# Performance work log

Measured on AMD Instinct MI355X. Metric: run time of the kernel, lower is better.

## Reference

```python
import jax, jax.numpy as jnp
import numpy as np

S, M, B, D, H, DH = 1024, 1024, 4, 1024, 16, 64
T = S + M
EPS = 1e-5


def setup_inputs() -> dict:
    key = jax.random.key(0)
    ks = jax.random.split(key, 6)
    x = jax.random.normal(ks[0], (S, B, D), dtype=jnp.float32)
    pos_emb = jax.random.normal(ks[1], (S, 1, D), dtype=jnp.float32)
    memory = jax.random.normal(ks[2], (M, B, D), dtype=jnp.float32)
    # causal mask: query i (global position M+i) cannot attend to key j > M+i
    i = jnp.arange(S)[:, None]
    j = jnp.arange(T)[None, :]
    mask = jnp.broadcast_to((j > (i + M))[:, :, None], (S, T, B))  # [S,T,B] bool
    w_qkv = jax.random.normal(ks[3], (D, 3 * H * DH), dtype=jnp.float32) * (D ** -0.5)
    w_o = jax.random.normal(ks[4], (H * DH, D), dtype=jnp.float32) * ((H * DH) ** -0.5)
    ln_gamma = jnp.ones((D,), dtype=jnp.float32)
    ln_beta = jnp.zeros((D,), dtype=jnp.float32)
    return {"x": x, "pos_emb": pos_emb, "memory": memory, "mask": mask,
            "w_qkv": w_qkv, "w_o": w_o, "ln_gamma": ln_gamma, "ln_beta": ln_beta}


def reference(x, pos_emb, memory, mask, w_qkv, w_o, ln_gamma, ln_beta):
    seq_len = x.shape[0]
    scale = 1.0 / (DH ** 0.5)
    x = x + pos_emb[-seq_len:]                      # [S,B,D]
    c = jnp.concatenate([memory, x], axis=0)        # [T,B,D]
    qkv = jnp.einsum('tbd,de->tbe', c, w_qkv)       # [T,B,3*H*DH]
    q, k, v = jnp.split(qkv, 3, axis=-1)
    q = q.reshape(-1, B, H, DH)[-seq_len:]          # [S,B,H,DH]
    k = k.reshape(-1, B, H, DH)                     # [T,B,H,DH]
    v = v.reshape(-1, B, H, DH)
    score = jnp.einsum('ibnd,jbnd->ijbn', q, k) * scale  # [S,T,B,H]
    score = jnp.where(mask[:, :, :, None], -jnp.inf, score)
    prob = jax.nn.softmax(score, axis=1)
    vec = jnp.einsum('ijbn,jbnd->ibnd', prob, v)    # [S,B,H,DH]
    vec = vec.reshape(seq_len, B, H * DH)
    attn_out = jnp.einsum('sbe,ed->sbd', vec, w_o)  # [S,B,D]
    y = x + attn_out
    mu = jnp.mean(y, axis=-1, keepdims=True)
    var = jnp.mean(jnp.square(y - mu), axis=-1, keepdims=True)
    out = (y - mu) * jax.lax.rsqrt(var + EPS) * ln_gamma + ln_beta
    return out
```

## Files before the change

### kernel.cpp

```cpp
#include <hip/hip_runtime.h>
#include <stdint.h>

#define S_  1024
#define M_  1024
#define B_  4
#define D_  1024
#define H_  16
#define DH_ 64
#define T_  2048

typedef __attribute__((ext_vector_type(8))) short bf8;
typedef __attribute__((ext_vector_type(4))) float f32x4;
typedef __attribute__((ext_vector_type(16))) float f32x16;
typedef __attribute__((ext_vector_type(8))) unsigned short u16x8;
typedef __attribute__((ext_vector_type(4))) unsigned short u16x4;
typedef __attribute__((ext_vector_type(4))) unsigned int u32x4;
typedef unsigned short u16;

#define MFMA(a, b, c)   __builtin_amdgcn_mfma_f32_16x16x32_bf16((a), (b), (c), 0, 0, 0)
#define MFMA32(a, b, c) __builtin_amdgcn_mfma_f32_32x32x16_bf16((a), (b), (c), 0, 0, 0)

static __device__ __forceinline__ u16 f2bf(float f) {
  unsigned int u = __builtin_bit_cast(unsigned int, f);
  u += 0x7fffu + ((u >> 16) & 1u);
  return (u16)(u >> 16);
}

static __device__ __forceinline__ void gload16(const void* g, void* l) {
  __builtin_amdgcn_global_load_lds((const __attribute__((address_space(1))) unsigned int*)g,
                                   (__attribute__((address_space(3))) unsigned int*)l,
                                   16, 0, 0);
}

static __device__ __forceinline__ float fexp2(float x) {
  return __builtin_amdgcn_exp2f(x);
}
static __device__ __forceinline__ unsigned int cvtpk(float lo, float hi) {
  unsigned int r; asm("v_cvt_pk_bf16_f32 %0, %1, %2" : "=v"(r) : "v"(lo), "v"(hi)); return r;
}
static __device__ __forceinline__ void plswap(unsigned int& a, unsigned int& b) {
  asm volatile("s_nop 1\n\tv_permlane32_swap_b32 %0, %1" : "+v"(a), "+v"(b));
}

__global__ __launch_bounds__(256) void k_prep(const float* __restrict__ x,
    const float* __restrict__ pos, const float* __restrict__ mem,
    u16* __restrict__ cbf, float* __restrict__ xp)
{
  const int gid = blockIdx.x * 256 + threadIdx.x;
  const int e = gid * 8;
  const int col = e & 1023;
  float4 v0, v1;
  if (e < M_ * B_ * D_) {
    v0 = *(const float4*)(mem + e);
    v1 = *(const float4*)(mem + e + 4);
  } else {
    const int i2 = e - M_ * B_ * D_;
    v0 = *(const float4*)(x + i2);
    v1 = *(const float4*)(x + i2 + 4);
    const int srow = i2 >> 12;
    const float4 p0 = *(const float4*)(pos + srow * 1024 + col);
    const float4 p1 = *(const float4*)(pos + srow * 1024 + col + 4);
    v0.x += p0.x; v0.y += p0.y; v0.z += p0.z; v0.w += p0.w;
    v1.x += p1.x; v1.y += p1.y; v1.z += p1.z; v1.w += p1.w;
    *(float4*)(xp + i2) = v0;
    *(float4*)(xp + i2 + 4) = v1;
  }
  u16x8 c;
  c[0] = f2bf(v0.x); c[1] = f2bf(v0.y); c[2] = f2bf(v0.z); c[3] = f2bf(v0.w);
  c[4] = f2bf(v1.x); c[5] = f2bf(v1.y); c[6] = f2bf(v1.z); c[7] = f2bf(v1.w);
  *(u16x8*)(cbf + e) = c;
}

__global__ __launch_bounds__(256) void k_wtrans(const float* __restrict__ src,
    u16* __restrict__ dst, int Rr, int Cc)
{
  __shared__ float tl[64][65];
  const int r0 = blockIdx.x * 64, c0 = blockIdx.y * 64;
  const int tid = threadIdx.x;
  const int lr = tid >> 4, lc = (tid & 15) * 4;
  for (int i = 0; i < 4; ++i) {
    const int rr = lr + i * 16;
    const float4 v = *(const float4*)(src + (size_t)(r0 + rr) * Cc + c0 + lc);
    tl[rr][lc] = v.x; tl[rr][lc + 1] = v.y; tl[rr][lc + 2] = v.z; tl[rr][lc + 3] = v.w;
  }
  __syncthreads();
  const int c = tid >> 2, k0 = (tid & 3) * 16;
  u16x8 a, b;
  for (int j = 0; j < 8; ++j) { a[j] = f2bf(tl[k0 + j][c]); b[j] = f2bf(tl[k0 + 8 + j][c]); }
  u16* dp = dst + (size_t)(c0 + c) * Rr + r0 + k0;
  *(u16x8*)dp = a;
  *(u16x8*)(dp + 8) = b;
}

#define STAGE_G(buf, kt) do { const int k0_ = (kt) * 32;                       \
    for (int s_ = 0; s_ < 2; ++s_) {                                           \
      const int rr_ = (wave * 2 + s_) * 16 + sr;                               \
      gload16(A + (size_t)(row0 + rr_) * 1024 + k0_ + sk,                      \
              &sA[buf][(wave * 2 + s_) * 512]);                                \
      gload16(Bt + (size_t)(col0 + rr_) * 1024 + k0_ + sk,                     \
              &sB[buf][(wave * 2 + s_) * 512]);                                \
    } } while (0)

#define GEMM_MAINLOOP()                                                        \
  STAGE_G(0, 0);                                                               \
  int cur = 0;                                                                 \
  for (int kt = 0; kt < 32; ++kt) {                                            \
    asm volatile("s_waitcnt vmcnt(0)" ::: "memory");                           \
    __syncthreads();                                                           \
    if (kt + 1 < 32) STAGE_G(cur ^ 1, kt + 1);                                 \
    bf8 af[4], bfv[4];                                                         \
    const u16* pa = &sA[cur][(wm + lrow) * 32 + lgrp * 8];                     \
    const u16* pb = &sB[cur][(wn + lrow) * 32 + lgrp * 8];                     \
    for (int i = 0; i < 4; ++i) af[i] = *(const bf8*)(pa + i * 512);           \
    for (int j = 0; j < 4; ++j) bfv[j] = *(const bf8*)(pb + j * 512);          \
    __builtin_amdgcn_s_setprio(1);                                             \
    for (int i = 0; i < 4; ++i)                                                \
      for (int j = 0; j < 4; ++j) acc[i][j] = MFMA(af[i], bfv[j], acc[i][j]);  \
    __builtin_amdgcn_s_setprio(0);                                             \
    cur ^= 1;                                                                  \
  }

__global__ __launch_bounds__(256) void k_gemm_qkvf(const u16* __restrict__ A,
    const u16* __restrict__ Bt, u16* __restrict__ Qd, u16* __restrict__ Kd,
    u16* __restrict__ VTd)
{
  __shared__ u16 sA[2][4096];
  __shared__ u16 sB[2][4096];
  const int tid = threadIdx.x, lane = tid & 63, wave = tid >> 6;
  const int lrow = lane & 15, lgrp = lane >> 4;
  const int wm = (wave >> 1) * 64, wn = (wave & 1) * 64;
  const int sr = lane >> 2, sk = (lane & 3) * 8;

  const int bid = blockIdx.x;
  const int lid = (bid & 7) * 160 + (bid >> 3);
  int rowb, colb;
  if (lid < 512) { rowb = lid >> 4; colb = 8 + (lid & 15); }
  else { const int l2 = lid - 512; const int q = l2 / 24; rowb = 32 + q; colb = l2 - q * 24; }
  const int row0 = rowb * 128, col0 = colb * 128;

  f32x4 acc[4][4];
  for (int i = 0; i < 4; ++i)
    for (int j = 0; j < 4; ++j) acc[i][j] = f32x4{0.f, 0.f, 0.f, 0.f};

  GEMM_MAINLOOP();

  const int which = col0 >> 10;
  for (int i = 0; i < 4; ++i)
    for (int j = 0; j < 4; ++j)
      for (int r = 0; r < 4; ++r) {
        const int grow = row0 + wm + i * 16 + lgrp * 4 + r;
        const int gcol = col0 + wn + j * 16 + lrow;
        const u16 bv = f2bf(acc[i][j][r]);
        const int t = grow >> 2, bb2 = grow & 3;
        const int rem = gcol & 1023;
        const int bh = bb2 * 16 + (rem >> 6), dh = rem & 63;
        if (which == 0) {
          if (t >= M_) Qd[((size_t)bh * S_ + (t - M_)) * 64 + dh] = bv;
        } else if (which == 1) {
          Kd[((size_t)bh * T_ + t) * 64 + (dh ^ ((t & 7) << 3))] = bv;
        } else {
          VTd[((size_t)bh * 64 + dh) * T_ + (t & ~63) + ((t & 63) ^ ((dh & 7) << 3))] = bv;
        }
      }
}

__global__ __launch_bounds__(256) void k_gemm_out(const u16* __restrict__ A,
    const u16* __restrict__ Bt, const float* __restrict__ xp,
    float* __restrict__ y)
{
  __shared__ u16 sA[2][2048];
  __shared__ u16 sB[2][4096];
  const int tid = threadIdx.x, lane = tid & 63, wave = tid >> 6;
  const int lrow = lane & 15, lgrp = lane >> 4;
  const int wm = (wave >> 1) * 32, wn = (wave & 1) * 64;
  const int row0 = blockIdx.y * 64, col0 = blockIdx.x * 128;
  const int sr = lane >> 2, sk = (lane & 3) * 8;

  f32x4 acc[2][4];
  for (int i = 0; i < 2; ++i)
    for (int j = 0; j < 4; ++j) acc[i][j] = f32x4{0.f, 0.f, 0.f, 0.f};

#define STAGE_O(buf, kt) do { const int k0_ = (kt) * 32;                       \
    const int rra_ = wave * 16 + sr;                                           \
    gload16(A + (size_t)(row0 + rra_) * 1024 + k0_ + sk,                       \
            &sA[buf][wave * 512]);                                             \
    for (int s_ = 0; s_ < 2; ++s_) {                                           \
      const int rrb_ = (wave * 2 + s_) * 16 + sr;                              \
      gload16(Bt + (size_t)(col0 + rrb_) * 1024 + k0_ + sk,                    \
              &sB[buf][(wave * 2 + s_) * 512]);                                \
    } } while (0)

  STAGE_O(0, 0);
  int cur = 0;
  for (int kt = 0; kt < 32; ++kt) {
    asm volatile("s_waitcnt vmcnt(0)" ::: "memory");
    __syncthreads();
    if (kt + 1 < 32) STAGE_O(cur ^ 1, kt + 1);
    bf8 af[2], bfv[4];
    const u16* pa = &sA[cur][(wm + lrow) * 32 + lgrp * 8];
    const u16* pb = &sB[cur][(wn + lrow) * 32 + lgrp * 8];
    for (int i = 0; i < 2; ++i) af[i] = *(const bf8*)(pa + i * 512);
    for (int j = 0; j < 4; ++j) bfv[j] = *(const bf8*)(pb + j * 512);
    __builtin_amdgcn_s_setprio(1);
    for (int i = 0; i < 2; ++i)
      for (int j = 0; j < 4; ++j) acc[i][j] = MFMA(af[i], bfv[j], acc[i][j]);
    __builtin_amdgcn_s_setprio(0);
    cur ^= 1;
  }

  for (int i = 0; i < 2; ++i)
    for (int j = 0; j < 4; ++j)
      for (int r = 0; r < 4; ++r) {
        const int grow = row0 + wm + i * 16 + lgrp * 4 + r;
        const int gcol = col0 + wn + j * 16 + lrow;
        y[(size_t)grow * 1024 + gcol] = acc[i][j][r] + xp[(size_t)grow * 1024 + gcol];
      }
}

__global__ __launch_bounds__(256) void k_attn(const u16* __restrict__ Qd,
    const u16* __restrict__ Kd, const u16* __restrict__ VTd,
    u16* __restrict__ vec)
{
  __shared__ u16 Kl[2][4096];
  __shared__ u16 Vl[2][4096];
  const int tid = threadIdx.x, lane = tid & 63, wave = tid >> 6;
  const int ql = lane & 31, hi = lane >> 5;
  const int qb = blockIdx.x, bh = blockIdx.y;
  const int bb = bh >> 4, hh = bh & 15;
  const int q0 = qb * 128 + wave * 32;
  const int myq = q0 + ql;
  const int klim = M_ + myq;

  bf8 qf[4];
  const u16* qrow = Qd + ((size_t)bh * S_ + myq) * 64 + hi * 8;
#pragma unroll
  for (int c = 0; c < 4; ++c) qf[c] = *(const bf8*)(qrow + c * 16);

  const u16* kb = Kd + (size_t)bh * T_ * 64;
  const u16* vb = VTd + (size_t)bh * 64 * T_;

  f32x16 o0, o1;
#pragma unroll
  for (int r = 0; r < 16; ++r) { o0[r] = 0.f; o1[r] = 0.f; }
  float m_run = 0.f, l_run = 0.f;
  const float cs = 0.125f * 1.44269504f;

  const int nkt = (M_ + qb * 128 + 128) >> 6;

  auto stage = [&](int buf, int kt) {
    const int t0 = kt * 64;
#pragma unroll
    for (int i = 0; i < 2; ++i) {
      const int ch = i * 256 + tid;
      gload16(kb + (size_t)t0 * 64 + ch * 8, &Kl[buf][ch * 8]);
    }
#pragma unroll
    for (int i = 0; i < 2; ++i) {
      const int ch = i * 256 + tid;
      gload16(vb + (size_t)(ch >> 3) * T_ + t0 + (ch & 7) * 8, &Vl[buf][ch * 8]);
    }
  };

  stage(0, 0);
  int cur = 0;
  for (int kt = 0; kt < nkt; ++kt) {
    if (kt + 1 < nkt) {
      stage(cur ^ 1, kt + 1);
      asm volatile("s_waitcnt vmcnt(4)" ::: "memory");
    } else {
      asm volatile("s_waitcnt vmcnt(0)" ::: "memory");
    }
    __builtin_amdgcn_s_barrier();

    const u16* Kc = Kl[cur];
    const u16* Vc = Vl[cur];

    f32x16 s0, s1;
#pragma unroll
    for (int r = 0; r < 16; ++r) { s0[r] = 0.f; s1[r] = 0.f; }
    const int tr0 = ql, tr1 = 32 + ql;
    const int sw0 = (tr0 & 7) << 3;
    __builtin_amdgcn_s_setprio(1);
#pragma unroll
    for (int c = 0; c < 4; ++c) {
      const int db = c * 16 + hi * 8;
      const bf8 ka = *(const bf8*)(Kc + tr0 * 64 + (db ^ sw0));
      const bf8 kbfr = *(const bf8*)(Kc + tr1 * 64 + (db ^ sw0));
      s0 = MFMA32(ka, qf[c], s0);
      s1 = MFMA32(kbfr, qf[c], s1);
    }
    __builtin_amdgcn_s_setprio(0);

    float p0[16], p1[16];
#pragma unroll
    for (int r = 0; r < 16; ++r) { p0[r] = s0[r] * cs; p1[r] = s1[r] * cs; }
    if (kt * 64 + 63 > M_ + q0) {
#pragma unroll
      for (int r = 0; r < 16; ++r) {
        const int kg = kt * 64 + (r & 3) + 8 * (r >> 2) + 4 * hi;
        if (kg > klim)      p0[r] = -1e30f;
        if (kg + 32 > klim) p1[r] = -1e30f;
      }
    }
    float mx = fmaxf(p0[0], p1[0]);
#pragma unroll
    for (int r = 1; r < 16; ++r) mx = fmaxf(mx, fmaxf(p0[r], p1[r]));
    mx = fmaxf(mx, __shfl_xor(mx, 32));
    if (__any(mx - m_run > 8.f)) {
      const float mnew = fmaxf(m_run, mx);
      const float al = fexp2(m_run - mnew);
      l_run *= al;
#pragma unroll
      for (int r = 0; r < 16; ++r) {
        const int qloc = (r & 3) + 8 * (r >> 2) + 4 * hi;
        const float ar = __shfl(al, (lane & 32) + qloc);
        o0[r] *= ar; o1[r] *= ar;
      }
      m_run = mnew;
    }
    float rs = 0.f;
#pragma unroll
    for (int r = 0; r < 16; ++r) {
      p0[r] = fexp2(p0[r] - m_run);
      p1[r] = fexp2(p1[r] - m_run);
      rs += p0[r] + p1[r];
    }
    rs += __shfl_xor(rs, 32);
    l_run += rs;

    bf8 paf[2][2];
    {
      unsigned int a0 = cvtpk(p0[0], p0[1]),  a1 = cvtpk(p0[2], p0[3]);
      unsigned int a2 = cvtpk(p0[4], p0[5]),  a3 = cvtpk(p0[6], p0[7]);
      unsigned int b0 = cvtpk(p0[8], p0[9]),  b1 = cvtpk(p0[10], p0[11]);
      unsigned int b2 = cvtpk(p0[12], p0[13]), b3 = cvtpk(p0[14], p0[15]);
      plswap(a0, a2); plswap(a1, a3); plswap(b0, b2); plswap(b1, b3);
      u32x4 f0 = {a0, a1, a2, a3}, f1 = {b0, b1, b2, b3};
      paf[0][0] = __builtin_bit_cast(bf8, f0);
      paf[0][1] = __builtin_bit_cast(bf8, f1);
    }
    {
      unsigned int a0 = cvtpk(p1[0], p1[1]),  a1 = cvtpk(p1[2], p1[3]);
      unsigned int a2 = cvtpk(p1[4], p1[5]),  a3 = cvtpk(p1[6], p1[7]);
      unsigned int b0 = cvtpk(p1[8], p1[9]),  b1 = cvtpk(p1[10], p1[11]);
      unsigned int b2 = cvtpk(p1[12], p1[13]), b3 = cvtpk(p1[14], p1[15]);
      plswap(a0, a2); plswap(a1, a3); plswap(b0, b2); plswap(b1, b3);
      u32x4 f0 = {a0, a1, a2, a3}, f1 = {b0, b1, b2, b3};
      paf[1][0] = __builtin_bit_cast(bf8, f0);
      paf[1][1] = __builtin_bit_cast(bf8, f1);
    }

    __builtin_amdgcn_s_setprio(1);
#pragma unroll
    for (int kc = 0; kc < 4; ++kc) {
      const int tb = kc * 16 + hi * 8;
      const bf8 pfrag = paf[kc >> 1][kc & 1];
      const int vr0 = ql, vr1 = 32 + ql;
      const bf8 vf0 = *(const bf8*)(Vc + vr0 * 64 + (tb ^ ((vr0 & 7) << 3)));
      const bf8 vf1 = *(const bf8*)(Vc + vr1 * 64 + (tb ^ ((vr1 & 7) << 3)));
      o0 = MFMA32(pfrag, vf0, o0);
      o1 = MFMA32(pfrag, vf1, o1);
    }
    __builtin_amdgcn_s_setprio(0);
    __builtin_amdgcn_s_barrier();
    cur ^= 1;
  }

  const float linv = 1.0f / l_run;
#pragma unroll
  for (int r = 0; r < 16; ++r) {
    const int qloc = (r & 3) + 8 * (r >> 2) + 4 * hi;
    const float li = __shfl(linv, (lane & 32) + qloc);
    const int srow = q0 + qloc;
    const size_t base = ((size_t)srow * B_ + bb) * 1024 + hh * 64;
    vec[base + ql]      = f2bf(o0[r] * li);
    vec[base + 32 + ql] = f2bf(o1[r] * li);
  }
}

__global__ __launch_bounds__(256) void k_ln(const float* __restrict__ y,
    const float* __restrict__ g, const float* __restrict__ be,
    float* __restrict__ out)
{
  const int row = blockIdx.x, tid = threadIdx.x;
  const float4 v = *(const float4*)(y + (size_t)row * 1024 + tid * 4);
  float s = v.x + v.y + v.z + v.w;
  float ss = v.x * v.x + v.y * v.y + v.z * v.z + v.w * v.w;
  for (int mk = 1; mk < 64; mk <<= 1) { s += __shfl_xor(s, mk); ss += __shfl_xor(ss, mk); }
  __shared__ float red[8];
  if ((tid & 63) == 0) { red[tid >> 6] = s; red[4 + (tid >> 6)] = ss; }
  __syncthreads();
  s = red[0] + red[1] + red[2] + red[3];
  ss = red[4] + red[5] + red[6] + red[7];
  const float mu = s * (1.0f / 1024.0f);
  const float var = ss * (1.0f / 1024.0f) - mu * mu;
  const float rstd = rsqrtf(var + 1e-5f);
  const float4 gg = *(const float4*)(g + tid * 4);
  const float4 bb = *(const float4*)(be + tid * 4);
  float4 o;
  o.x = (v.x - mu) * rstd * gg.x + bb.x;
  o.y = (v.y - mu) * rstd * gg.y + bb.y;
  o.z = (v.z - mu) * rstd * gg.z + bb.z;
  o.w = (v.w - mu) * rstd * gg.w + bb.w;
  *(float4*)(out + (size_t)row * 1024 + tid * 4) = o;
}

extern "C" void kernel_launch(void* const* d_in, const int* in_sizes, int n_in,
                              void* d_out, int out_size, void* d_ws, size_t ws_size,
                              hipStream_t stream)
{
  const float* x     = (const float*)d_in[0];
  const float* pos   = (const float*)d_in[1];
  const float* mem   = (const float*)d_in[2];
  const float* wqkv  = (const float*)d_in[4];
  const float* wo    = (const float*)d_in[5];
  const float* gamma = (const float*)d_in[6];
  const float* beta  = (const float*)d_in[7];
  float* out = (float*)d_out;

  if (ws_size < ((size_t)104 << 20)) return;

  char* ws = (char*)d_ws;
  u16*   cbf = (u16*)(ws + 0);
  float* y   = (float*)(ws + 0);
  float* xp  = (float*)(ws + ((size_t)16 << 20));
  u16*   wqt = (u16*)(ws + ((size_t)32 << 20));
  u16*   wot = (u16*)(ws + ((size_t)38 << 20));
  u16*   Qd  = (u16*)(ws + ((size_t)40 << 20));
  u16*   Kd  = (u16*)(ws + ((size_t)48 << 20));
  u16*   VTd = (u16*)(ws + ((size_t)80 << 20));
  u16*   vec = (u16*)(ws + ((size_t)96 << 20));

  k_prep<<<4096, 256, 0, stream>>>(x, pos, mem, cbf, xp);
  k_wtrans<<<dim3(16, 48), 256, 0, stream>>>(wqkv, wqt, 1024, 3072);
  k_wtrans<<<dim3(16, 16), 256, 0, stream>>>(wo, wot, 1024, 1024);
  k_gemm_qkvf<<<1280, 256, 0, stream>>>(cbf, wqt, Qd, Kd, VTd);
  k_attn<<<dim3(8, 64), 256, 0, stream>>>(Qd, Kd, VTd, vec);
  k_gemm_out<<<dim3(8, 64), 256, 0, stream>>>(vec, wot, xp, y);
  k_ln<<<4096, 256, 0, stream>>>(y, gamma, beta, out);
}
```

Baseline: 199.8 us.

## Rewrite QKV GEMM with 128x256 tiles, triple-buffered LDS, pre-swizzled operands

The QKV projection GEMM now uses 128x256 output tiles (half as many blocks), a three-stage LDS ring with split A/B loads interleaved between two MFMA phases, and explicit barriers and sched_barriers. The prep and weight-transpose kernels write activations and weights with a 16-byte chunk XOR swizzle, so direct global-to-LDS loads land in an order that avoids LDS bank conflicts on the fragment reads. This aims to hide global latency and raise MFMA density. In exchange it raises register and LDS use per block, and the tile remap has to cover the skipped Q rows for memory tokens correctly.

```diff
diff --git a/kernel.cpp b/kernel.cpp
--- a/kernel.cpp
+++ b/kernel.cpp
@@ -48,7 +48,7 @@
 {
   const int gid = blockIdx.x * 256 + threadIdx.x;
   const int e = gid * 8;
-  const int col = e & 1023;
+  const int row = e >> 10, col = e & 1023;
   float4 v0, v1;
   if (e < M_ * B_ * D_) {
     v0 = *(const float4*)(mem + e);
@@ -68,11 +68,13 @@
   u16x8 c;
   c[0] = f2bf(v0.x); c[1] = f2bf(v0.y); c[2] = f2bf(v0.z); c[3] = f2bf(v0.w);
   c[4] = f2bf(v1.x); c[5] = f2bf(v1.y); c[6] = f2bf(v1.z); c[7] = f2bf(v1.w);
-  *(u16x8*)(cbf + e) = c;
+  const int ch = col >> 3;
+  const int chs = (ch & ~3) | ((ch & 3) ^ (row & 3));
+  *(u16x8*)(cbf + (size_t)row * 1024 + chs * 8) = c;
 }
 
 __global__ __launch_bounds__(256) void k_wtrans(const float* __restrict__ src,
-    u16* __restrict__ dst, int Rr, int Cc)
+    u16* __restrict__ dst, int Rr, int Cc, int swz)
 {
   __shared__ float tl[64][65];
   const int r0 = blockIdx.x * 64, c0 = blockIdx.y * 64;
@@ -87,69 +89,114 @@
   const int c = tid >> 2, k0 = (tid & 3) * 16;
   u16x8 a, b;
   for (int j = 0; j < 8; ++j) { a[j] = f2bf(tl[k0 + j][c]); b[j] = f2bf(tl[k0 + 8 + j][c]); }
-  u16* dp = dst + (size_t)(c0 + c) * Rr + r0 + k0;
-  *(u16x8*)dp = a;
-  *(u16x8*)(dp + 8) = b;
-}
-
-#define STAGE_G(buf, kt) do { const int k0_ = (kt) * 32;                       \
-    for (int s_ = 0; s_ < 2; ++s_) {                                           \
-      const int rr_ = (wave * 2 + s_) * 16 + sr;                               \
-      gload16(A + (size_t)(row0 + rr_) * 1024 + k0_ + sk,                      \
-              &sA[buf][(wave * 2 + s_) * 512]);                                \
-      gload16(Bt + (size_t)(col0 + rr_) * 1024 + k0_ + sk,                     \
-              &sB[buf][(wave * 2 + s_) * 512]);                                \
-    } } while (0)
-
-#define GEMM_MAINLOOP()                                                        \
-  STAGE_G(0, 0);                                                               \
-  int cur = 0;                                                                 \
-  for (int kt = 0; kt < 32; ++kt) {                                            \
-    asm volatile("s_waitcnt vmcnt(0)" ::: "memory");                           \
-    __syncthreads();                                                           \
-    if (kt + 1 < 32) STAGE_G(cur ^ 1, kt + 1);                                 \
-    bf8 af[4], bfv[4];                                                         \
-    const u16* pa = &sA[cur][(wm + lrow) * 32 + lgrp * 8];                     \
-    const u16* pb = &sB[cur][(wn + lrow) * 32 + lgrp * 8];                     \
-    for (int i = 0; i < 4; ++i) af[i] = *(const bf8*)(pa + i * 512);           \
-    for (int j = 0; j < 4; ++j) bfv[j] = *(const bf8*)(pb + j * 512);          \
-    __builtin_amdgcn_s_setprio(1);                                             \
-    for (int i = 0; i < 4; ++i)                                                \
-      for (int j = 0; j < 4; ++j) acc[i][j] = MFMA(af[i], bfv[j], acc[i][j]);  \
-    __builtin_amdgcn_s_setprio(0);                                             \
-    cur ^= 1;                                                                  \
-  }
-
-__global__ __launch_bounds__(256) void k_gemm_qkvf(const u16* __restrict__ A,
+  const int roww = c0 + c;
+  int ch0 = (r0 + k0) >> 3, ch1 = ch0 + 1;
+  if (swz) {
+    const int sx = roww & 3;
+    ch0 = (ch0 & ~3) | ((ch0 & 3) ^ sx);
+    ch1 = (ch1 & ~3) | ((ch1 & 3) ^ sx);
+  }
+  u16* dp = dst + (size_t)roww * Rr;
+  *(u16x8*)(dp + ch0 * 8) = a;
+  *(u16x8*)(dp + ch1 * 8) = b;
+}
+
+__global__ __launch_bounds__(256, 2) void k_gemm_qkv3(const u16* __restrict__ Aa,
     const u16* __restrict__ Bt, u16* __restrict__ Qd, u16* __restrict__ Kd,
     u16* __restrict__ VTd)
 {
-  __shared__ u16 sA[2][4096];
-  __shared__ u16 sB[2][4096];
+  __shared__ u16 lds[3][12288];
   const int tid = threadIdx.x, lane = tid & 63, wave = tid >> 6;
   const int lrow = lane & 15, lgrp = lane >> 4;
-  const int wm = (wave >> 1) * 64, wn = (wave & 1) * 64;
-  const int sr = lane >> 2, sk = (lane & 3) * 8;
+  const int wr = wave >> 1, wc = wave & 1;
 
   const int bid = blockIdx.x;
-  const int lid = (bid & 7) * 160 + (bid >> 3);
+  const int lid = (bid & 7) * 80 + (bid >> 3);
   int rowb, colb;
-  if (lid < 512) { rowb = lid >> 4; colb = 8 + (lid & 15); }
-  else { const int l2 = lid - 512; const int q = l2 / 24; rowb = 32 + q; colb = l2 - q * 24; }
-  const int row0 = rowb * 128, col0 = colb * 128;
-
-  f32x4 acc[4][4];
+  if (lid < 128) { rowb = 32 + (lid >> 2); colb = lid & 3; }
+  else { const int l2 = lid - 128; rowb = l2 >> 3; colb = 4 + (l2 & 7); }
+  const int row0 = rowb * 128, col0 = colb * 256;
+
+  f32x4 acc[4][8];
+#pragma unroll
   for (int i = 0; i < 4; ++i)
-    for (int j = 0; j < 4; ++j) acc[i][j] = f32x4{0.f, 0.f, 0.f, 0.f};
-
-  GEMM_MAINLOOP();
+#pragma unroll
+    for (int j = 0; j < 8; ++j) acc[i][j] = f32x4{0.f, 0.f, 0.f, 0.f};
+
+  bf8 a_[4], b_[4];
+
+#define STA3(bufi, kt) do {                                                    \
+    _Pragma("unroll") for (int s_ = 0; s_ < 2; ++s_) {                         \
+      const int ca_ = tid + s_ * 256;                                          \
+      gload16(Aa + (size_t)(row0 + (ca_ >> 2)) * 1024 + (kt) * 32 + (ca_ & 3) * 8, \
+              &lds[bufi][ca_ * 8]);                                            \
+    } } while (0)
+
+#define STB3(bufi, kt) do {                                                    \
+    _Pragma("unroll") for (int s_ = 0; s_ < 4; ++s_) {                         \
+      const int cb_ = tid + s_ * 256;                                          \
+      gload16(Bt + (size_t)(col0 + (cb_ >> 2)) * 1024 + (kt) * 32 + (cb_ & 3) * 8, \
+              &lds[bufi][4096 + cb_ * 8]);                                     \
+    } } while (0)
+
+#define LDA3(bufi) do {                                                        \
+    _Pragma("unroll") for (int i_ = 0; i_ < 4; ++i_) {                         \
+      const int r_ = wr * 64 + i_ * 16 + lrow;                                 \
+      a_[i_] = *(const bf8*)&lds[bufi][r_ * 32 + ((lgrp ^ (r_ & 3)) << 3)];    \
+    } } while (0)
+
+#define LDB3(bufi, ph) do {                                                    \
+    _Pragma("unroll") for (int j_ = 0; j_ < 4; ++j_) {                         \
+      const int r_ = wc * 128 + ((ph) * 4 + j_) * 16 + lrow;                   \
+      b_[j_] = *(const bf8*)&lds[bufi][4096 + r_ * 32 + ((lgrp ^ (r_ & 3)) << 3)]; \
+    } } while (0)
+
+#define MM3(ph) do {                                                           \
+    _Pragma("unroll") for (int i_ = 0; i_ < 4; ++i_)                           \
+    _Pragma("unroll") for (int j_ = 0; j_ < 4; ++j_)                           \
+      acc[i_][(ph) * 4 + j_] = MFMA(a_[i_], b_[j_], acc[i_][(ph) * 4 + j_]);   \
+  } while (0)
+
+  STA3(0, 0); STB3(0, 0); STA3(1, 1); STB3(1, 1);
+  asm volatile("s_waitcnt vmcnt(6)" ::: "memory");
+  __builtin_amdgcn_s_barrier();
+
+  int c0 = 0;
+#pragma unroll 1
+  for (int t = 0; t < 32; ++t) {
+    const int c2 = (c0 + 2 >= 3) ? c0 - 1 : c0 + 2;
+    LDA3(c0); LDB3(c0, 0);
+    if (t <= 29) STA3(c2, t + 2);
+    __builtin_amdgcn_s_barrier();
+    __builtin_amdgcn_sched_barrier(0);
+    __builtin_amdgcn_s_setprio(1);
+    MM3(0);
+    __builtin_amdgcn_s_setprio(0);
+    __builtin_amdgcn_sched_barrier(0);
+    __builtin_amdgcn_s_barrier();
+    LDB3(c0, 1);
+    if (t <= 29) STB3(c2, t + 2);
+    __builtin_amdgcn_s_barrier();
+    __builtin_amdgcn_sched_barrier(0);
+    __builtin_amdgcn_s_setprio(1);
+    MM3(1);
+    __builtin_amdgcn_s_setprio(0);
+    __builtin_amdgcn_sched_barrier(0);
+    if (t < 30) { asm volatile("s_waitcnt vmcnt(6)" ::: "memory"); }
+    else        { asm volatile("s_waitcnt vmcnt(0)" ::: "memory"); }
+    __builtin_amdgcn_s_barrier();
+    c0 = (c0 == 2) ? 0 : c0 + 1;
+  }
 
   const int which = col0 >> 10;
+#pragma unroll
   for (int i = 0; i < 4; ++i)
-    for (int j = 0; j < 4; ++j)
+#pragma unroll
+    for (int j = 0; j < 8; ++j)
+#pragma unroll
       for (int r = 0; r < 4; ++r) {
-        const int grow = row0 + wm + i * 16 + lgrp * 4 + r;
-        const int gcol = col0 + wn + j * 16 + lrow;
+        const int grow = row0 + wr * 64 + i * 16 + lgrp * 4 + r;
+        const int gcol = col0 + wc * 128 + j * 16 + lrow;
         const u16 bv = f2bf(acc[i][j][r]);
         const int t = grow >> 2, bb2 = grow & 3;
         const int rem = gcol & 1023;
@@ -432,9 +479,9 @@
   u16*   vec = (u16*)(ws + ((size_t)96 << 20));
 
   k_prep<<<4096, 256, 0, stream>>>(x, pos, mem, cbf, xp);
-  k_wtrans<<<dim3(16, 48), 256, 0, stream>>>(wqkv, wqt, 1024, 3072);
-  k_wtrans<<<dim3(16, 16), 256, 0, stream>>>(wo, wot, 1024, 1024);
-  k_gemm_qkvf<<<1280, 256, 0, stream>>>(cbf, wqt, Qd, Kd, VTd);
+  k_wtrans<<<dim3(16, 48), 256, 0, stream>>>(wqkv, wqt, 1024, 3072, 1);
+  k_wtrans<<<dim3(16, 16), 256, 0, stream>>>(wo, wot, 1024, 1024, 0);
+  k_gemm_qkv3<<<640, 256, 0, stream>>>(cbf, wqt, Qd, Kd, VTd);
   k_attn<<<dim3(8, 64), 256, 0, stream>>>(Qd, Kd, VTd, vec);
   k_gemm_out<<<dim3(8, 64), 256, 0, stream>>>(vec, wot, xp, y);
   k_ln<<<4096, 256, 0, stream>>>(y, gamma, beta, out);
```

Measured after the change: 200.8 us. Within noise of the previous version (+0.5%).

## Triple-buffer QKV GEMM loads and pre-swizzle operands to avoid LDS conflicts

Applied to the files above, without the earlier changes.

The QKV projection GEMM moves from double to triple buffering, keeping two k-tiles of global-to-LDS loads in flight with a partial vmcnt wait. The prep and weight-transpose kernels now write the bf16 activations and QKV weights with an XOR chunk swizzle, and the GEMM reads LDS through the matching pattern. This is meant to hide global load latency and cut LDS bank conflicts on the fragment reads. It costs more shared memory per block, with a launch-bounds hint aiming for 3 blocks per CU. The old shared GEMM macros are removed, which breaks compilation if the hidden output GEMM still uses them.

```diff
diff --git a/kernel.cpp b/kernel.cpp
--- a/kernel.cpp
+++ b/kernel.cpp
@@ -20,6 +20,8 @@
 #define MFMA(a, b, c)   __builtin_amdgcn_mfma_f32_16x16x32_bf16((a), (b), (c), 0, 0, 0)
 #define MFMA32(a, b, c) __builtin_amdgcn_mfma_f32_32x32x16_bf16((a), (b), (c), 0, 0, 0)
 
+#define SIG(r) ((((r) >> 1) ^ ((r) >> 3)) & 3)
+
 static __device__ __forceinline__ u16 f2bf(float f) {
   unsigned int u = __builtin_bit_cast(unsigned int, f);
   u += 0x7fffu + ((u >> 16) & 1u);
@@ -48,7 +50,7 @@
 {
   const int gid = blockIdx.x * 256 + threadIdx.x;
   const int e = gid * 8;
-  const int col = e & 1023;
+  const int row = e >> 10, col = e & 1023;
   float4 v0, v1;
   if (e < M_ * B_ * D_) {
     v0 = *(const float4*)(mem + e);
@@ -68,11 +70,13 @@
   u16x8 c;
   c[0] = f2bf(v0.x); c[1] = f2bf(v0.y); c[2] = f2bf(v0.z); c[3] = f2bf(v0.w);
   c[4] = f2bf(v1.x); c[5] = f2bf(v1.y); c[6] = f2bf(v1.z); c[7] = f2bf(v1.w);
-  *(u16x8*)(cbf + e) = c;
+  const int ch = col >> 3;
+  const int chs = (ch & ~3) | ((ch & 3) ^ SIG(row));
+  *(u16x8*)(cbf + (size_t)row * 1024 + chs * 8) = c;
 }
 
 __global__ __launch_bounds__(256) void k_wtrans(const float* __restrict__ src,
-    u16* __restrict__ dst, int Rr, int Cc)
+    u16* __restrict__ dst, int Rr, int Cc, int swz)
 {
   __shared__ float tl[64][65];
   const int r0 = blockIdx.x * 64, c0 = blockIdx.y * 64;
@@ -87,45 +91,24 @@
   const int c = tid >> 2, k0 = (tid & 3) * 16;
   u16x8 a, b;
   for (int j = 0; j < 8; ++j) { a[j] = f2bf(tl[k0 + j][c]); b[j] = f2bf(tl[k0 + 8 + j][c]); }
-  u16* dp = dst + (size_t)(c0 + c) * Rr + r0 + k0;
-  *(u16x8*)dp = a;
-  *(u16x8*)(dp + 8) = b;
-}
-
-#define STAGE_G(buf, kt) do { const int k0_ = (kt) * 32;                       \
-    for (int s_ = 0; s_ < 2; ++s_) {                                           \
-      const int rr_ = (wave * 2 + s_) * 16 + sr;                               \
-      gload16(A + (size_t)(row0 + rr_) * 1024 + k0_ + sk,                      \
-              &sA[buf][(wave * 2 + s_) * 512]);                                \
-      gload16(Bt + (size_t)(col0 + rr_) * 1024 + k0_ + sk,                     \
-              &sB[buf][(wave * 2 + s_) * 512]);                                \
-    } } while (0)
-
-#define GEMM_MAINLOOP()                                                        \
-  STAGE_G(0, 0);                                                               \
-  int cur = 0;                                                                 \
-  for (int kt = 0; kt < 32; ++kt) {                                            \
-    asm volatile("s_waitcnt vmcnt(0)" ::: "memory");                           \
-    __syncthreads();                                                           \
-    if (kt + 1 < 32) STAGE_G(cur ^ 1, kt + 1);                                 \
-    bf8 af[4], bfv[4];                                                         \
-    const u16* pa = &sA[cur][(wm + lrow) * 32 + lgrp * 8];                     \
-    const u16* pb = &sB[cur][(wn + lrow) * 32 + lgrp * 8];                     \
-    for (int i = 0; i < 4; ++i) af[i] = *(const bf8*)(pa + i * 512);           \
-    for (int j = 0; j < 4; ++j) bfv[j] = *(const bf8*)(pb + j * 512);          \
-    __builtin_amdgcn_s_setprio(1);                                             \
-    for (int i = 0; i < 4; ++i)                                                \
-      for (int j = 0; j < 4; ++j) acc[i][j] = MFMA(af[i], bfv[j], acc[i][j]);  \
-    __builtin_amdgcn_s_setprio(0);                                             \
-    cur ^= 1;                                                                  \
-  }
-
-__global__ __launch_bounds__(256) void k_gemm_qkvf(const u16* __restrict__ A,
+  const int roww = c0 + c;
+  int ch0 = (r0 + k0) >> 3, ch1 = ((r0 + k0) >> 3) + 1;
+  if (swz) {
+    const int sx = SIG(roww);
+    ch0 = (ch0 & ~3) | ((ch0 & 3) ^ sx);
+    ch1 = (ch1 & ~3) | ((ch1 & 3) ^ sx);
+  }
+  u16* dp = dst + (size_t)roww * Rr;
+  *(u16x8*)(dp + ch0 * 8) = a;
+  *(u16x8*)(dp + ch1 * 8) = b;
+}
+
+__global__ __launch_bounds__(256, 3) void k_gemm_qkvs(const u16* __restrict__ A,
     const u16* __restrict__ Bt, u16* __restrict__ Qd, u16* __restrict__ Kd,
     u16* __restrict__ VTd)
 {
-  __shared__ u16 sA[2][4096];
-  __shared__ u16 sB[2][4096];
+  __shared__ u16 sA[3][4096];
+  __shared__ u16 sB[3][4096];
   const int tid = threadIdx.x, lane = tid & 63, wave = tid >> 6;
   const int lrow = lane & 15, lgrp = lane >> 4;
   const int wm = (wave >> 1) * 64, wn = (wave & 1) * 64;
@@ -139,14 +122,57 @@
   const int row0 = rowb * 128, col0 = colb * 128;
 
   f32x4 acc[4][4];
+#pragma unroll
   for (int i = 0; i < 4; ++i)
+#pragma unroll
     for (int j = 0; j < 4; ++j) acc[i][j] = f32x4{0.f, 0.f, 0.f, 0.f};
 
-  GEMM_MAINLOOP();
+#define STAGE_S(bufi, kt) do { const int k0_ = (kt) * 32;                      \
+    _Pragma("unroll") for (int s_ = 0; s_ < 2; ++s_) {                         \
+      const int rr_ = (wave * 2 + s_) * 16 + sr;                               \
+      gload16(A + (size_t)(row0 + rr_) * 1024 + k0_ + sk,                      \
+              &sA[bufi][(wave * 2 + s_) * 512]);                               \
+      gload16(Bt + (size_t)(col0 + rr_) * 1024 + k0_ + sk,                     \
+              &sB[bufi][(wave * 2 + s_) * 512]);                               \
+    } } while (0)
+
+  STAGE_S(0, 0); STAGE_S(1, 1);
+
+  int c0 = 0;
+#pragma unroll 1
+  for (int t = 0; t < 32; ++t) {
+    if (t < 31) { asm volatile("s_waitcnt vmcnt(4)" ::: "memory"); }
+    else        { asm volatile("s_waitcnt vmcnt(0)" ::: "memory"); }
+    __builtin_amdgcn_s_barrier();
+    __builtin_amdgcn_sched_barrier(0);
+    const int c2 = (c0 + 2 >= 3) ? c0 - 1 : c0 + 2;
+    if (t <= 29) STAGE_S(c2, t + 2);
+    bf8 af[4], bfv[4];
+#pragma unroll
+    for (int i = 0; i < 4; ++i) {
+      const int r_ = wm + i * 16 + lrow;
+      af[i] = *(const bf8*)&sA[c0][r_ * 32 + ((lgrp ^ SIG(r_)) << 3)];
+    }
+#pragma unroll
+    for (int j = 0; j < 4; ++j) {
+      const int r_ = wn + j * 16 + lrow;
+      bfv[j] = *(const bf8*)&sB[c0][r_ * 32 + ((lgrp ^ SIG(r_)) << 3)];
+    }
+    __builtin_amdgcn_s_setprio(1);
+#pragma unroll
+    for (int i = 0; i < 4; ++i)
+#pragma unroll
+      for (int j = 0; j < 4; ++j) acc[i][j] = MFMA(af[i], bfv[j], acc[i][j]);
+    __builtin_amdgcn_s_setprio(0);
+    c0 = (c0 == 2) ? 0 : c0 + 1;
+  }
 
   const int which = col0 >> 10;
+#pragma unroll
   for (int i = 0; i < 4; ++i)
+#pragma unroll
     for (int j = 0; j < 4; ++j)
+#pragma unroll
       for (int r = 0; r < 4; ++r) {
         const int grow = row0 + wm + i * 16 + lgrp * 4 + r;
         const int gcol = col0 + wn + j * 16 + lrow;
@@ -432,9 +458,9 @@
   u16*   vec = (u16*)(ws + ((size_t)96 << 20));
 
   k_prep<<<4096, 256, 0, stream>>>(x, pos, mem, cbf, xp);
-  k_wtrans<<<dim3(16, 48), 256, 0, stream>>>(wqkv, wqt, 1024, 3072);
-  k_wtrans<<<dim3(16, 16), 256, 0, stream>>>(wo, wot, 1024, 1024);
-  k_gemm_qkvf<<<1280, 256, 0, stream>>>(cbf, wqt, Qd, Kd, VTd);
+  k_wtrans<<<dim3(16, 48), 256, 0, stream>>>(wqkv, wqt, 1024, 3072, 1);
+  k_wtrans<<<dim3(16, 16), 256, 0, stream>>>(wo, wot, 1024, 1024, 0);
+  k_gemm_qkvs<<<1280, 256, 0, stream>>>(cbf, wqt, Qd, Kd, VTd);
   k_attn<<<dim3(8, 64), 256, 0, stream>>>(Qd, Kd, VTd, vec);
   k_gemm_out<<<dim3(8, 64), 256, 0, stream>>>(vec, wot, xp, y);
   k_ln<<<4096, 256, 0, stream>>>(y, gamma, beta, out);
```

After: 199.6 us. No clear change (-0.1%).
